# Optimization experiments

Hardware: AMD Instinct MI355X
Metric: run time of the kernel (lower is better)

The kernel has to match this reference:

```python
import jax, jax.numpy as jnp
import numpy as np

N_NODES = 100000
N_EDGES = 1600000
IN_CH = 512
MID_CH = 64   # hard-coded mid_layer_channel in the module
OUT_CH = 40


def setup_inputs() -> dict:
    key = jax.random.key(0)
    k0, k1, k2, k3 = jax.random.split(key, 4)
    node_feature = jax.random.normal(k0, (N_NODES, IN_CH), dtype=jnp.float32)
    # edge index [2, E]: row 0 = src, row 1 = dst
    adj_list = jax.random.randint(k1, (2, N_EDGES), 0, N_NODES, dtype=jnp.int32)
    # GCNConv parameters (Glorot-ish scale)
    W1 = jax.random.normal(k2, (IN_CH, MID_CH), dtype=jnp.float32) * (1.0 / np.sqrt(IN_CH))
    b1 = jnp.zeros((MID_CH,), dtype=jnp.float32)
    W2 = jax.random.normal(k3, (MID_CH, OUT_CH), dtype=jnp.float32) * (1.0 / np.sqrt(MID_CH))
    b2 = jnp.zeros((OUT_CH,), dtype=jnp.float32)
    return {"node_feature": node_feature, "adj_list": adj_list,
            "W1": W1, "b1": b1, "W2": W2, "b2": b2}


def _gcn_conv(x, W, b, src, dst, deg_inv_sqrt, n_nodes):
    # Standard GCNConv: D^{-1/2} (A + I) D^{-1/2} (x W) + b
    h = x @ W                                             # [N, F_out]
    norm = deg_inv_sqrt[src] * deg_inv_sqrt[dst]          # [E]
    agg = jax.ops.segment_sum(h[src] * norm[:, None], dst, num_segments=n_nodes)
    agg = agg + h * (deg_inv_sqrt * deg_inv_sqrt)[:, None]  # self-loop term
    return agg + b


def reference(node_feature, adj_list, W1, b1, W2, b2):
    n = node_feature.shape[0]
    src, dst = adj_list[0], adj_list[1]
    # degree with self-loops (in-degree at dst + 1)
    deg = jax.ops.segment_sum(jnp.ones_like(dst, dtype=node_feature.dtype), dst,
                              num_segments=n) + 1.0
    deg_inv_sqrt = jax.lax.rsqrt(deg)
    h = jax.nn.elu(_gcn_conv(node_feature, W1, b1, src, dst, deg_inv_sqrt, n))
    out = _gcn_conv(h, W2, b2, src, dst, deg_inv_sqrt, n)
    return jax.nn.log_softmax(out, axis=1)
```

## Files before the change

kernel.cpp:

```cpp
#include <hip/hip_runtime.h>
#include <hip/hip_bf16.h>
#include <math.h>

#define IN_CH 512
#define MID_CH 64
#define OUT_CH 40

typedef __attribute__((ext_vector_type(8))) short short8;
typedef __attribute__((ext_vector_type(4))) float f32x4;
typedef __attribute__((ext_vector_type(2))) float f32x2;

static __device__ __forceinline__ unsigned short f2bf(float f) {
    unsigned int u = __float_as_uint(f);
    u += 0x7fffu + ((u >> 16) & 1u);
    return (unsigned short)(u >> 16);
}

__global__ void k_count(const int* __restrict__ dst, int* __restrict__ cnt, int E) {
    int pb = blockIdx.x & 7;
    int ch = blockIdx.x >> 3;
    int nch = gridDim.x >> 3;
    int ech = (E + nch - 1) / nch;
    int e0 = ch * ech;
    int e1 = e0 + ech; if (e1 > E) e1 = E;
    for (int e = e0 + threadIdx.x; e < e1; e += blockDim.x) {
        int d = dst[e];
        if ((d & 7) == pb) atomicAdd(&cnt[d], 1);
    }
}

__global__ void k_scanA(const int* __restrict__ cnt, int* __restrict__ rowptr,
                        int* __restrict__ bsum, float* __restrict__ dis, int N) {
    __shared__ int wsum[16];
    int i = blockIdx.x * 1024 + threadIdx.x;
    int lane = threadIdx.x & 63, wv = threadIdx.x >> 6;
    int v = (i < N) ? cnt[i] : 0;
    if (i < N) dis[i] = rsqrtf((float)v + 1.0f);
    int x = (v + 3) & ~3;
    #pragma unroll
    for (int off = 1; off < 64; off <<= 1) {
        int t = __shfl_up(x, off);
        if (lane >= off) x += t;
    }
    if (lane == 63) wsum[wv] = x;
    __syncthreads();
    if (wv == 0 && lane < 16) {
        int own = wsum[lane];
        int y = own;
        #pragma unroll
        for (int off = 1; off < 16; off <<= 1) {
            int t = __shfl_up(y, off);
            if (lane >= off) y += t;
        }
        wsum[lane] = y - own;
        if (lane == 15) bsum[blockIdx.x] = y;
    }
    __syncthreads();
    if (i < N) rowptr[i + 1] = x + wsum[wv];
}

__global__ void k_scanB(int* __restrict__ bsum, int nb) {
    __shared__ int tmp[2];
    int lane = threadIdx.x & 63, wv = threadIdx.x >> 6;
    int v = (threadIdx.x < nb) ? bsum[threadIdx.x] : 0;
    int x = v;
    #pragma unroll
    for (int off = 1; off < 64; off <<= 1) {
        int t = __shfl_up(x, off);
        if (lane >= off) x += t;
    }
    if (lane == 63) tmp[wv] = x;
    __syncthreads();
    int add = (wv == 1) ? tmp[0] : 0;
    if (threadIdx.x < nb) bsum[threadIdx.x] = x - v + add;
}

__global__ void k_scanC(int* __restrict__ rowptr, const int* __restrict__ bsum, int N) {
    int i = blockIdx.x * 1024 + threadIdx.x;
    if (i < N) rowptr[i + 1] += bsum[blockIdx.x];
    if (i == 0) rowptr[0] = 0;
}

__global__ void k_padfill(int* __restrict__ esrc, int dummy_off, int total) {
    int i = blockIdx.x * blockDim.x + threadIdx.x;
    if (i < total) esrc[i] = dummy_off;
}

__global__ void k_prepw(const float* __restrict__ W1, unsigned short* __restrict__ w1f) {
    int f = blockIdx.x * 256 + threadIdx.x;
    int k = f >> 6, c = f & 63;
    w1f[(((k >> 3) * 64) + c) * 8 + (k & 7)] = f2bf(W1[f]);
}

__launch_bounds__(512, 2)
__global__ void k_fillgemm(const float* __restrict__ X, const unsigned short* __restrict__ w1f,
                           const float* __restrict__ dis, unsigned char* __restrict__ h1q,
                           int N, int FB,
                           const int* __restrict__ src, const int* __restrict__ dst,
                           const int* __restrict__ rowptr, int* __restrict__ cur,
                           int* __restrict__ esrc, int E) {
    __shared__ __align__(16) unsigned short wlds[IN_CH * MID_CH];
    int b = blockIdx.x;
    int gb, fb = -1;
    if (b < 2 * FB) { if (b & 1) { fb = b >> 1; gb = -1; } else gb = b >> 1; }
    else gb = b - FB;

    if (fb >= 0) {
        int pb = fb & 7;
        int ch = fb >> 3;
        int nch = FB >> 3;
        int ech = (E + nch - 1) / nch;
        int e0 = ch * ech;
        int e1 = e0 + ech; if (e1 > E) e1 = E;
        for (int e = e0 + (int)threadIdx.x; e < e1; e += 512) {
            int d = dst[e];
            if ((d & 7) == pb) {
                int p = rowptr[d] + atomicAdd(&cur[d], 1);
                esrc[p] = src[e] << 6;
            }
        }
        return;
    }

    {
        const uint4* s4 = (const uint4*)w1f;
        uint4* d4 = (uint4*)wlds;
        #pragma unroll
        for (int i = 0; i < 8; ++i)
            d4[threadIdx.x + i * 512] = s4[threadIdx.x + i * 512];
    }
    __syncthreads();

    int wave = threadIdx.x >> 6, lane = threadIdx.x & 63;
    int rbase = gb * 128 + wave * 16;
    int g = lane >> 4;
    int arow = rbase + (lane & 15);
    if (arow > N - 1) arow = N - 1;
    const float* xp = X + (size_t)arow * IN_CH + g * 8;

    f32x4 acc[4];
    #pragma unroll
    for (int i = 0; i < 4; ++i) acc[i] = (f32x4){0.f, 0.f, 0.f, 0.f};

    float4 bx0[2], bx1[2];
    {
        const float4* p0 = (const float4*)(xp);
        const float4* p1 = (const float4*)(xp + 32);
        bx0[0] = p0[0]; bx1[0] = p0[1];
        bx0[1] = p1[0]; bx1[1] = p1[1];
    }

    #pragma unroll
    for (int ks = 0; ks < 16; ++ks) {
        float4 x0 = bx0[ks & 1], x1 = bx1[ks & 1];
        if (ks < 14) {
            const float4* p = (const float4*)(xp + (ks + 2) * 32);
            bx0[ks & 1] = p[0]; bx1[ks & 1] = p[1];
        }
        short8 a;
        a[0] = (short)f2bf(x0.x); a[1] = (short)f2bf(x0.y);
        a[2] = (short)f2bf(x0.z); a[3] = (short)f2bf(x0.w);
        a[4] = (short)f2bf(x1.x); a[5] = (short)f2bf(x1.y);
        a[6] = (short)f2bf(x1.z); a[7] = (short)f2bf(x1.w);

        int cibase = (ks * 4 + g) * 64 + (lane & 15);
        #pragma unroll
        for (int ct = 0; ct < 4; ++ct) {
            short8 bfr = *((const short8*)(wlds + (size_t)(cibase + ct * 16) * 8));
            acc[ct] = __builtin_amdgcn_mfma_f32_16x16x32_bf16(a, bfr, acc[ct], 0, 0, 0);
        }
    }

    int colb = lane & 15;
    int rquad = rbase + (lane >> 4) * 4;
    #pragma unroll
    for (int ct = 0; ct < 4; ++ct) {
        #pragma unroll
        for (int r = 0; r < 4; ++r) {
            int row = rquad + r;
            if (row < N) {
                float v = acc[ct][r] * dis[row];
                unsigned q = __builtin_amdgcn_cvt_pk_fp8_f32(v, v, 0, false);
                h1q[(size_t)row * 64 + ct * 16 + colb] = (unsigned char)q;
            }
        }
    }
}

#define AGG_UNPACK8(Q)                                              \
    {                                                               \
        f32x2 lo_ = __builtin_amdgcn_cvt_pk_f32_fp8((Q), false);    \
        f32x2 hi_ = __builtin_amdgcn_cvt_pk_f32_fp8((Q), true);     \
        acc[0] += lo_[0]; acc[1] += lo_[1];                         \
        acc[2] += hi_[0]; acc[3] += hi_[1];                         \
    }

__launch_bounds__(256)
__global__ void k_agg1(const unsigned char* __restrict__ hq, const float* __restrict__ dis,
                       const int* __restrict__ rowptr, const int* __restrict__ esrc,
                       const float* __restrict__ b1, unsigned char* __restrict__ h2q,
                       int N) {
    int wv = threadIdx.x >> 6, lane = threadIdx.x & 63;
    int n = blockIdx.x * 4 + wv;
    if (n >= N) return;
    int g = lane >> 4, cg = lane & 15;
    int beg = rowptr[n], end = rowptr[n + 1];
    unsigned cgoff = (unsigned)(cg * 4);
    const char* hb = (const char*)hq;

    f32x4 acc = (f32x4){0.f, 0.f, 0.f, 0.f};
    for (int cbeg = beg; cbeg < end; cbeg += 64) {
        int m = end - cbeg; if (m > 64) m = 64;
        int soff = esrc[cbeg + lane];
        int k4n = m >> 2;
        int k4 = 0;
        for (; k4 + 4 <= k4n; k4 += 4) {
            int o0 = __shfl(soff, (k4 + 0) * 4 + g);
            int o1 = __shfl(soff, (k4 + 1) * 4 + g);
            int o2 = __shfl(soff, (k4 + 2) * 4 + g);
            int o3 = __shfl(soff, (k4 + 3) * 4 + g);
            unsigned q0 = *(const unsigned*)(hb + ((unsigned)o0 + cgoff));
            unsigned q1 = *(const unsigned*)(hb + ((unsigned)o1 + cgoff));
            unsigned q2 = *(const unsigned*)(hb + ((unsigned)o2 + cgoff));
            unsigned q3 = *(const unsigned*)(hb + ((unsigned)o3 + cgoff));
            AGG_UNPACK8(q0) AGG_UNPACK8(q1) AGG_UNPACK8(q2) AGG_UNPACK8(q3)
        }
        for (; k4 < k4n; ++k4) {
            int o = __shfl(soff, k4 * 4 + g);
            unsigned q = *(const unsigned*)(hb + ((unsigned)o + cgoff));
            AGG_UNPACK8(q)
        }
    }
    #pragma unroll
    for (int off = 32; off >= 16; off >>= 1) {
        acc[0] += __shfl_xor(acc[0], off);
        acc[1] += __shfl_xor(acc[1], off);
        acc[2] += __shfl_xor(acc[2], off);
        acc[3] += __shfl_xor(acc[3], off);
    }
    if (g == 0) {
        float dn = dis[n];
        unsigned qs = *(const unsigned*)(hb + ((unsigned)(n * 64) + cgoff));
        f32x2 slo = __builtin_amdgcn_cvt_pk_f32_fp8(qs, false);
        f32x2 shi = __builtin_amdgcn_cvt_pk_f32_fp8(qs, true);
        float4 b4 = *(const float4*)(b1 + cg * 4);
        float v0 = dn * (acc[0] + slo[0]) + b4.x;
        float v1 = dn * (acc[1] + slo[1]) + b4.y;
        float v2 = dn * (acc[2] + shi[0]) + b4.z;
        float v3 = dn * (acc[3] + shi[1]) + b4.w;
        v0 = v0 > 0.f ? v0 : expm1f(v0);
        v1 = v1 > 0.f ? v1 : expm1f(v1);
        v2 = v2 > 0.f ? v2 : expm1f(v2);
        v3 = v3 > 0.f ? v3 : expm1f(v3);
        unsigned w = __builtin_amdgcn_cvt_pk_fp8_f32(dn * v0, dn * v1, 0, false);
        w = __builtin_amdgcn_cvt_pk_fp8_f32(dn * v2, dn * v3, w, true);
        *(unsigned*)(h2q + (size_t)n * 64 + cg * 4) = w;
    }
}

__launch_bounds__(256)
__global__ void k_agg2(const unsigned char* __restrict__ hq, const float* __restrict__ dis,
                       const int* __restrict__ rowptr, const int* __restrict__ esrc,
                       const float* __restrict__ W2, const float* __restrict__ b2,
                       float* __restrict__ out, int N) {
    __shared__ float w2l[MID_CH * OUT_CH];
    __shared__ float vl[4 * MID_CH];
    for (int f = threadIdx.x; f < MID_CH * OUT_CH; f += 256) w2l[f] = W2[f];
    __syncthreads();

    int wv = threadIdx.x >> 6, lane = threadIdx.x & 63;
    int n = blockIdx.x * 4 + wv;
    if (n >= N) return;
    int g = lane >> 4, cg = lane & 15;
    int beg = rowptr[n], end = rowptr[n + 1];
    unsigned cgoff = (unsigned)(cg * 4);
    const char* hb = (const char*)hq;

    f32x4 acc = (f32x4){0.f, 0.f, 0.f, 0.f};
    for (int cbeg = beg; cbeg < end; cbeg += 64) {
        int m = end - cbeg; if (m > 64) m = 64;
        int soff = esrc[cbeg + lane];
        int k4n = m >> 2;
        int k4 = 0;
        for (; k4 + 4 <= k4n; k4 += 4) {
            int o0 = __shfl(soff, (k4 + 0) * 4 + g);
            int o1 = __shfl(soff, (k4 + 1) * 4 + g);
            int o2 = __shfl(soff, (k4 + 2) * 4 + g);
            int o3 = __shfl(soff, (k4 + 3) * 4 + g);
            unsigned q0 = *(const unsigned*)(hb + ((unsigned)o0 + cgoff));
            unsigned q1 = *(const unsigned*)(hb + ((unsigned)o1 + cgoff));
            unsigned q2 = *(const unsigned*)(hb + ((unsigned)o2 + cgoff));
            unsigned q3 = *(const unsigned*)(hb + ((unsigned)o3 + cgoff));
            AGG_UNPACK8(q0) AGG_UNPACK8(q1) AGG_UNPACK8(q2) AGG_UNPACK8(q3)
        }
        for (; k4 < k4n; ++k4) {
            int o = __shfl(soff, k4 * 4 + g);
            unsigned q = *(const unsigned*)(hb + ((unsigned)o + cgoff));
            AGG_UNPACK8(q)
        }
    }
    #pragma unroll
    for (int off = 32; off >= 16; off >>= 1) {
        acc[0] += __shfl_xor(acc[0], off);
        acc[1] += __shfl_xor(acc[1], off);
        acc[2] += __shfl_xor(acc[2], off);
        acc[3] += __shfl_xor(acc[3], off);
    }
    if (g == 0) {
        float dn = dis[n];
        unsigned qs = *(const unsigned*)(hb + ((unsigned)(n * 64) + cgoff));
        f32x2 slo = __builtin_amdgcn_cvt_pk_f32_fp8(qs, false);
        f32x2 shi = __builtin_amdgcn_cvt_pk_f32_fp8(qs, true);
        float4 v;
        v.x = dn * (acc[0] + slo[0]);
        v.y = dn * (acc[1] + slo[1]);
        v.z = dn * (acc[2] + shi[0]);
        v.w = dn * (acc[3] + shi[1]);
        *(float4*)&vl[wv * 64 + cg * 4] = v;
    }

    float o = (lane < OUT_CH) ? b2[lane] : 0.f;
    const float* vrow = &vl[wv * 64];
    #pragma unroll 8
    for (int c = 0; c < MID_CH; ++c)
        o += vrow[c] * w2l[c * OUT_CH + lane];

    float mx = (lane < OUT_CH) ? o : -1e30f;
    #pragma unroll
    for (int off = 32; off > 0; off >>= 1) mx = fmaxf(mx, __shfl_xor(mx, off));
    float e = (lane < OUT_CH) ? expf(o - mx) : 0.f;
    float ssum = e;
    #pragma unroll
    for (int off = 32; off > 0; off >>= 1) ssum += __shfl_xor(ssum, off);
    if (lane < OUT_CH)
        out[(size_t)n * OUT_CH + lane] = o - mx - logf(ssum);
}

extern "C" void kernel_launch(void* const* d_in, const int* in_sizes, int n_in,
                              void* d_out, int out_size, void* d_ws, size_t ws_size,
                              hipStream_t stream) {
    const float* X  = (const float*)d_in[0];
    const int* adj  = (const int*)d_in[1];
    const float* W1 = (const float*)d_in[2];
    const float* b1 = (const float*)d_in[3];
    const float* W2 = (const float*)d_in[4];
    const float* b2 = (const float*)d_in[5];
    float* out = (float*)d_out;

    int N = in_sizes[0] / IN_CH;
    int E = in_sizes[1] / 2;
    const int* srcp = adj;
    const int* dstp = adj + E;
    int nchunk = (N + 1023) / 1024;
    int epad_max = E + 3 * N + 128;
    int GB = (N + 127) / 128;
    int FB = 512;

    char* ws = (char*)d_ws;
    size_t off = 0;
    int*   cnt    = (int*)(ws + off);  off += (size_t)N * sizeof(int);
    float* dis    = (float*)(ws + off); off += (size_t)N * sizeof(float);
    int*   rowptr = (int*)(ws + off);  off += ((size_t)N + 8) * sizeof(int);
    int*   bsum   = (int*)(ws + off);  off += 128 * sizeof(int);
    int*   esrc   = (int*)(ws + off);  off += (size_t)epad_max * sizeof(int);
    unsigned short* w1f = (unsigned short*)(ws + off); off += (size_t)IN_CH * MID_CH * sizeof(unsigned short);
    unsigned char* h1q = (unsigned char*)(ws + off); off += (size_t)(N + 4) * MID_CH;
    unsigned char* h2q = (unsigned char*)(ws + off); off += (size_t)(N + 4) * MID_CH;

    hipMemsetAsync(cnt, 0, (size_t)N * sizeof(int), stream);
    k_prepw<<<(IN_CH * MID_CH + 255) / 256, 256, 0, stream>>>(W1, w1f);
    k_count<<<512, 256, 0, stream>>>(dstp, cnt, E);
    k_scanA<<<nchunk, 1024, 0, stream>>>(cnt, rowptr, bsum, dis, N);
    k_scanB<<<1, 128, 0, stream>>>(bsum, nchunk);
    k_scanC<<<nchunk, 1024, 0, stream>>>(rowptr, bsum, N);
    k_padfill<<<(epad_max + 255) / 256, 256, 0, stream>>>(esrc, N << 6, epad_max);
    hipMemsetAsync(cnt, 0, (size_t)N * sizeof(int), stream);
    hipMemsetAsync(h1q + (size_t)N * 64, 0, 64, stream);
    hipMemsetAsync(h2q + (size_t)N * 64, 0, 64, stream);

    k_fillgemm<<<GB + FB, 512, 0, stream>>>(X, w1f, dis, h1q, N, FB,
                                            srcp, dstp, rowptr, cnt, esrc, E);
    k_agg1<<<(N + 3) / 4, 256, 0, stream>>>(h1q, dis, rowptr, esrc, b1, h2q, N);
    k_agg2<<<(N + 3) / 4, 256, 0, stream>>>(h2q, dis, rowptr, esrc, W2, b2, out, N);
}
```

Baseline: 345.9 us.

## Split fused fill+GEMM kernel, prefill cursor with rowptr, read W1 from global

```diff
diff --git a/kernel.cpp b/kernel.cpp
--- a/kernel.cpp
+++ b/kernel.cpp
@@ -75,15 +75,38 @@
     if (threadIdx.x < nb) bsum[threadIdx.x] = x - v + add;
 }
 
-__global__ void k_scanC(int* __restrict__ rowptr, const int* __restrict__ bsum, int N) {
+__global__ void k_scanC(int* __restrict__ rowptr, int* __restrict__ cur,
+                        const int* __restrict__ bsum, int N) {
     int i = blockIdx.x * 1024 + threadIdx.x;
-    if (i < N) rowptr[i + 1] += bsum[blockIdx.x];
-    if (i == 0) rowptr[0] = 0;
+    if (i < N) {
+        int v = rowptr[i + 1] + bsum[blockIdx.x];
+        rowptr[i + 1] = v;
+        cur[i + 1] = v;
+    }
+    if (i == 0) { rowptr[0] = 0; cur[0] = 0; }
 }
 
 __global__ void k_padfill(int* __restrict__ esrc, int dummy_off, int total) {
     int i = blockIdx.x * blockDim.x + threadIdx.x;
     if (i < total) esrc[i] = dummy_off;
+}
+
+__global__ void k_fill(const int* __restrict__ src, const int* __restrict__ dst,
+                       int* __restrict__ cur, int* __restrict__ esrc, int E) {
+    int pb = blockIdx.x & 7;
+    int ch = blockIdx.x >> 3;
+    int nch = gridDim.x >> 3;
+    int ech = (E + nch - 1) / nch;
+    int e0 = ch * ech;
+    int e1 = e0 + ech; if (e1 > E) e1 = E;
+    #pragma unroll 4
+    for (int e = e0 + (int)threadIdx.x; e < e1; e += blockDim.x) {
+        int d = dst[e];
+        if ((d & 7) == pb) {
+            int p = atomicAdd(&cur[d], 1);
+            esrc[p] = src[e] << 6;
+        }
+    }
 }
 
 __global__ void k_prepw(const float* __restrict__ W1, unsigned short* __restrict__ w1f) {
@@ -92,51 +115,17 @@
     w1f[(((k >> 3) * 64) + c) * 8 + (k & 7)] = f2bf(W1[f]);
 }
 
-__launch_bounds__(512, 2)
-__global__ void k_fillgemm(const float* __restrict__ X, const unsigned short* __restrict__ w1f,
-                           const float* __restrict__ dis, unsigned char* __restrict__ h1q,
-                           int N, int FB,
-                           const int* __restrict__ src, const int* __restrict__ dst,
-                           const int* __restrict__ rowptr, int* __restrict__ cur,
-                           int* __restrict__ esrc, int E) {
-    __shared__ __align__(16) unsigned short wlds[IN_CH * MID_CH];
-    int b = blockIdx.x;
-    int gb, fb = -1;
-    if (b < 2 * FB) { if (b & 1) { fb = b >> 1; gb = -1; } else gb = b >> 1; }
-    else gb = b - FB;
-
-    if (fb >= 0) {
-        int pb = fb & 7;
-        int ch = fb >> 3;
-        int nch = FB >> 3;
-        int ech = (E + nch - 1) / nch;
-        int e0 = ch * ech;
-        int e1 = e0 + ech; if (e1 > E) e1 = E;
-        for (int e = e0 + (int)threadIdx.x; e < e1; e += 512) {
-            int d = dst[e];
-            if ((d & 7) == pb) {
-                int p = rowptr[d] + atomicAdd(&cur[d], 1);
-                esrc[p] = src[e] << 6;
-            }
-        }
-        return;
-    }
-
-    {
-        const uint4* s4 = (const uint4*)w1f;
-        uint4* d4 = (uint4*)wlds;
-        #pragma unroll
-        for (int i = 0; i < 8; ++i)
-            d4[threadIdx.x + i * 512] = s4[threadIdx.x + i * 512];
-    }
-    __syncthreads();
-
+__launch_bounds__(256, 6)
+__global__ void k_gemm1(const float* __restrict__ X, const unsigned short* __restrict__ w1f,
+                        const float* __restrict__ dis, unsigned char* __restrict__ h1q,
+                        int N) {
     int wave = threadIdx.x >> 6, lane = threadIdx.x & 63;
-    int rbase = gb * 128 + wave * 16;
+    int rbase = blockIdx.x * 64 + wave * 16;
     int g = lane >> 4;
     int arow = rbase + (lane & 15);
     if (arow > N - 1) arow = N - 1;
     const float* xp = X + (size_t)arow * IN_CH + g * 8;
+    const short8* wb = (const short8*)w1f;
 
     f32x4 acc[4];
     #pragma unroll
@@ -166,8 +155,8 @@
         int cibase = (ks * 4 + g) * 64 + (lane & 15);
         #pragma unroll
         for (int ct = 0; ct < 4; ++ct) {
-            short8 bfr = *((const short8*)(wlds + (size_t)(cibase + ct * 16) * 8));
-            acc[ct] = __builtin_amdgcn_mfma_f32_16x16x32_bf16(a, bfr, acc[ct], 0, 0, 0);
+            short8 b = wb[cibase + ct * 16];
+            acc[ct] = __builtin_amdgcn_mfma_f32_16x16x32_bf16(a, b, acc[ct], 0, 0, 0);
         }
     }
 
@@ -353,12 +342,11 @@
     const int* dstp = adj + E;
     int nchunk = (N + 1023) / 1024;
     int epad_max = E + 3 * N + 128;
-    int GB = (N + 127) / 128;
-    int FB = 512;
 
     char* ws = (char*)d_ws;
     size_t off = 0;
     int*   cnt    = (int*)(ws + off);  off += (size_t)N * sizeof(int);
+    int*   cur    = (int*)(ws + off);  off += ((size_t)N + 8) * sizeof(int);
     float* dis    = (float*)(ws + off); off += (size_t)N * sizeof(float);
     int*   rowptr = (int*)(ws + off);  off += ((size_t)N + 8) * sizeof(int);
     int*   bsum   = (int*)(ws + off);  off += 128 * sizeof(int);
@@ -372,14 +360,13 @@
     k_count<<<512, 256, 0, stream>>>(dstp, cnt, E);
     k_scanA<<<nchunk, 1024, 0, stream>>>(cnt, rowptr, bsum, dis, N);
     k_scanB<<<1, 128, 0, stream>>>(bsum, nchunk);
-    k_scanC<<<nchunk, 1024, 0, stream>>>(rowptr, bsum, N);
+    k_scanC<<<nchunk, 1024, 0, stream>>>(rowptr, cur, bsum, N);
     k_padfill<<<(epad_max + 255) / 256, 256, 0, stream>>>(esrc, N << 6, epad_max);
-    hipMemsetAsync(cnt, 0, (size_t)N * sizeof(int), stream);
     hipMemsetAsync(h1q + (size_t)N * 64, 0, 64, stream);
     hipMemsetAsync(h2q + (size_t)N * 64, 0, 64, stream);
 
-    k_fillgemm<<<GB + FB, 512, 0, stream>>>(X, w1f, dis, h1q, N, FB,
-                                            srcp, dstp, rowptr, cnt, esrc, E);
+    k_fill<<<1024, 256, 0, stream>>>(srcp, dstp, cur, esrc, E);
+    k_gemm1<<<(N + 63) / 64, 256, 0, stream>>>(X, w1f, dis, h1q, N);
     k_agg1<<<(N + 3) / 4, 256, 0, stream>>>(h1q, dis, rowptr, esrc, b1, h2q, N);
     k_agg2<<<(N + 3) / 4, 256, 0, stream>>>(h2q, dis, rowptr, esrc, W2, b2, out, N);
 }
```

Result: faster. 336.9 us (-2.6%).
